# Performance work log

Hardware: AMD Instinct MI355X
Metric: run time of the kernel (lower is better)

## Reference

```python
import jax, jax.numpy as jnp
import numpy as np

EMBED_DIM = 768
NUM_HEADS = 12
HEAD_DIM = EMBED_DIM // NUM_HEADS


def setup_inputs() -> dict:
    key = jax.random.key(0)
    k_x, k_wqkv, k_bqkv, k_wo, k_bo = jax.random.split(key, 5)
    B, S, D = 4, 2048, EMBED_DIM
    bound = 1.0 / np.sqrt(D)
    x = jax.random.normal(k_x, (B, S, D), dtype=jnp.float32)
    # nn.Linear weights: torch stores [out, in]; we keep same layout and use x @ W.T
    W_qkv = jax.random.uniform(k_wqkv, (3 * D, D), jnp.float32, -bound, bound)
    b_qkv = jax.random.uniform(k_bqkv, (3 * D,), jnp.float32, -bound, bound)
    W_out = jax.random.uniform(k_wo, (D, D), jnp.float32, -bound, bound)
    b_out = jax.random.uniform(k_bo, (D,), jnp.float32, -bound, bound)
    return {"x": x, "W_qkv": W_qkv, "b_qkv": b_qkv, "W_out": W_out, "b_out": b_out}


def reference(x, W_qkv, b_qkv, W_out, b_out):
    B, S, D = x.shape
    H, Hd = NUM_HEADS, HEAD_DIM
    qkv = x @ W_qkv.T + b_qkv                       # [B,S,3D]
    qkv = qkv.reshape(B, S, H, 3 * Hd).transpose(0, 2, 1, 3)  # [B,H,S,3Hd]
    q, k, v = jnp.split(qkv, 3, axis=-1)            # each [B,H,S,Hd]
    scale = Hd ** -0.5
    scores = jnp.einsum("bhsd,bhtd->bhst", q, k) * scale  # [B,H,S,S]
    weights = jax.nn.softmax(scores, axis=-1)
    ctx = jnp.einsum("bhst,bhtd->bhsd", weights, v)       # [B,H,S,Hd]
    ctx = ctx.transpose(0, 2, 1, 3).reshape(B, S, D)      # [B,S,D]
    return ctx @ W_out.T + b_out
```

## Files before the change

kernel.cpp:

```cpp
#include <hip/hip_runtime.h>
#include <hip/hip_bf16.h>
#include <stdint.h>
#include <math.h>

typedef unsigned short u16;
typedef __attribute__((ext_vector_type(8))) short short8;
typedef __attribute__((ext_vector_type(4))) short short4v;
typedef __attribute__((ext_vector_type(4))) float f32x4;
typedef __attribute__((ext_vector_type(16))) float f32x16;
typedef __attribute__((ext_vector_type(4))) unsigned int u32x4;
typedef __attribute__((ext_vector_type(2))) unsigned int u32x2;

#define NB 4
#define NS 2048
#define NH 12
#define HD 64
#define ND 768
#define ND3 2304

#define QSCALE 0.18033688f

__device__ __forceinline__ u16 f2bf(float f) {
    unsigned int u = __float_as_uint(f);
    unsigned int r = u + 0x7fffu + ((u >> 16) & 1u);
    return (u16)(r >> 16);
}

__device__ __forceinline__ void gload16(const u16* g, u16* s) {
    __builtin_amdgcn_global_load_lds(
        (const __attribute__((address_space(1))) unsigned int*)(const void*)g,
        (__attribute__((address_space(3))) unsigned int*)(void*)s, 16, 0, 0);
}

#define XN4   1572864
#define WQN4  442368
#define WON4  147456
__global__ __launch_bounds__(256) void castall(const float* __restrict__ x,
                                               const float* __restrict__ wq,
                                               const float* __restrict__ wo,
                                               u16* __restrict__ xb,
                                               u16* __restrict__ wqb,
                                               u16* __restrict__ wob) {
    int i = blockIdx.x * 256 + threadIdx.x;
    const float* s; u16* d; int j;
    if (i < XN4) { s = x; d = xb; j = i; }
    else if (i < XN4 + WQN4) { s = wq; d = wqb; j = i - XN4; }
    else if (i < XN4 + WQN4 + WON4) { s = wo; d = wob; j = i - XN4 - WQN4; }
    else return;
    float4 v = ((const float4*)s)[j];
    ushort4 o;
    o.x = f2bf(v.x); o.y = f2bf(v.y); o.z = f2bf(v.z); o.w = f2bf(v.w);
    ((ushort4*)d)[j] = o;
}

__global__ __launch_bounds__(256, 3) void gemm_qkv(const u16* __restrict__ A,
                                                   const u16* __restrict__ Bw,
                                                   const float* __restrict__ bias,
                                                   u16* __restrict__ Qg,
                                                   u16* __restrict__ Kg,
                                                   u16* __restrict__ Vtg) {
    __shared__ u16 lds[2][10240];
    const int tid = threadIdx.x;
    const int w = tid >> 6, l = tid & 63;
    const int lam = l & 15, quad = l >> 4;
    const int wm = w >> 1, wn = w & 1;
    const int bm = blockIdx.x * 128;
    const int hh = blockIdx.y;
    const int bn = hh * 192;
    const int K = ND;

    f32x4 acc[4][6];
#pragma unroll
    for (int i = 0; i < 4; i++)
#pragma unroll
        for (int j = 0; j < 6; j++) { f32x4 z = {0.f, 0.f, 0.f, 0.f}; acc[i][j] = z; }

    const u16* gp[5];
    int so[5];
#pragma unroll
    for (int i = 0; i < 5; i++) {
        int c = w * 5 + i;
        if (c < 8) { gp[i] = A + (size_t)(bm + c * 16 + lam) * K + quad * 8; so[i] = c * 512; }
        else { int nf = c - 8; gp[i] = Bw + (size_t)(bn + nf * 16 + lam) * K + quad * 8; so[i] = 4096 + nf * 512; }
    }

#pragma unroll
    for (int i = 0; i < 5; i++) gload16(gp[i], &lds[0][so[i]]);
    asm volatile("s_waitcnt vmcnt(0)" ::: "memory");
    __syncthreads();

    int cur = 0;
    for (int k0 = 0; k0 < K; k0 += 32) {
        if (k0 + 32 < K) {
#pragma unroll
            for (int i = 0; i < 5; i++) gload16(gp[i] + k0 + 32, &lds[cur ^ 1][so[i]]);
        }
        short8 a[4];
#pragma unroll
        for (int i = 0; i < 4; i++) a[i] = *(const short8*)(&lds[cur][(wm * 4 + i) * 512 + l * 8]);
#pragma unroll
        for (int half = 0; half < 2; half++) {
            short8 b[3];
#pragma unroll
            for (int j = 0; j < 3; j++) b[j] = *(const short8*)(&lds[cur][4096 + (wn * 6 + half * 3 + j) * 512 + l * 8]);
#pragma unroll
            for (int mf = 0; mf < 4; mf++)
#pragma unroll
                for (int j = 0; j < 3; j++)
                    acc[mf][half * 3 + j] = __builtin_amdgcn_mfma_f32_16x16x32_bf16(a[mf], b[j], acc[mf][half * 3 + j], 0, 0, 0);
        }
        asm volatile("s_waitcnt vmcnt(0)" ::: "memory");
        __syncthreads();
        cur ^= 1;
    }

#pragma unroll
    for (int nf = 0; nf < 6; nf++) {
        int nloc = wn * 96 + nf * 16;
        int rgn = nloc / 64;
        int d = (nloc % 64) + lam;
        float bv = bias[bn + nloc + lam];
        if (rgn == 2) {
#pragma unroll
            for (int mf = 0; mf < 4; mf++) {
                int m0 = bm + wm * 64 + mf * 16 + quad * 4;
                int bq = m0 >> 11, s0 = m0 & 2047;
                ushort4 o;
                o.x = f2bf(acc[mf][nf][0] + bv);
                o.y = f2bf(acc[mf][nf][1] + bv);
                o.z = f2bf(acc[mf][nf][2] + bv);
                o.w = f2bf(acc[mf][nf][3] + bv);
                *(ushort4*)(Vtg + ((size_t)((bq * NH + hh) * HD + d)) * NS + s0) = o;
            }
        } else {
            u16* dst = (rgn == 0) ? Qg : Kg;
            const float sc = (rgn == 0) ? QSCALE : 1.0f;
#pragma unroll
            for (int mf = 0; mf < 4; mf++)
#pragma unroll
                for (int r = 0; r < 4; r++) {
                    int m = bm + wm * 64 + mf * 16 + quad * 4 + r;
                    int bq = m >> 11, s = m & 2047;
                    dst[((size_t)((bq * NH + hh) * NS + s)) * HD + d] = f2bf((acc[mf][nf][r] + bv) * sc);
                }
        }
    }
}

__global__ __launch_bounds__(256, 3) void attn(const u16* __restrict__ Qg,
                                               const u16* __restrict__ Kg,
                                               const u16* __restrict__ Vtg,
                                               u16* __restrict__ ctx) {
    __shared__ u16 kt_lds[8192];
    __shared__ u16 vt_lds[8192];
    __shared__ float linv[128];
    const int tid = threadIdx.x;
    const int w = tid >> 6, L = tid & 63;
    const int r5 = L & 31, h = L >> 5;
    const int bid = blockIdx.x;
    const int qt = bid / 48, bh = bid % 48;
    const int b = bh / NH, hd = bh % NH;
    const u16* Qh = Qg + (size_t)bh * NS * HD;
    const u16* Kh = Kg + (size_t)bh * NS * HD;
    const u16* Vh = Vtg + (size_t)bh * HD * NS;

    const int qbase = qt * 128 + w * 32;

    short8 qf[4];
#pragma unroll
    for (int s = 0; s < 4; s++)
        qf[s] = *(const short8*)(Qh + (size_t)(qbase + r5) * HD + s * 16 + h * 8);

    f32x16 ot[2];
#pragma unroll
    for (int hg = 0; hg < 2; hg++)
#pragma unroll
        for (int r = 0; r < 16; r++) ot[hg][r] = 0.f;
    float lacc = 0.f;

    const u16* gp[8];
    u16* sp[8];
    int step;
    if (w < 2) {
#pragma unroll
        for (int i = 0; i < 8; i++) {
            int c = w * 8 + i, kg = c >> 2, s = c & 3;
            gp[i] = Kh + (size_t)(kg * 32 + r5) * HD + s * 16 + h * 8;
            sp[i] = kt_lds + c * 512;
        }
        step = 128 * HD;
    } else {
#pragma unroll
        for (int i = 0; i < 8; i++) {
            int c = (w - 2) * 8 + i;
            gp[i] = Vh + (size_t)((c >> 3) * 32 + r5) * NS + (c & 7) * 16 + h * 8;
            sp[i] = vt_lds + c * 512;
        }
        step = 128;
    }

    u32x4 rg[8];
#pragma unroll
    for (int i = 0; i < 8; i++) { rg[i] = *(const u32x4*)gp[i]; gp[i] += step; }

    for (int kt = 0; kt < 16; kt++) {
        __syncthreads();
#pragma unroll
        for (int i = 0; i < 8; i++) *(u32x4*)(sp[i] + (size_t)L * 8) = rg[i];
        __syncthreads();

        if (kt < 15) {
#pragma unroll
            for (int i = 0; i < 8; i++) { rg[i] = *(const u32x4*)gp[i]; gp[i] += step; }
        }

#pragma unroll
        for (int kg = 0; kg < 4; kg++) {
            f32x16 st;
#pragma unroll
            for (int r = 0; r < 16; r++) st[r] = 0.f;
#pragma unroll
            for (int s = 0; s < 4; s++) {
                short8 kf = *(const short8*)(kt_lds + (kg * 4 + s) * 512 + L * 8);
                st = __builtin_amdgcn_mfma_f32_32x32x16_bf16(kf, qf[s], st, 0, 0, 0);
            }

            unsigned int q8[8];
#pragma unroll
            for (int i = 0; i < 8; i++) {
                float e0 = __builtin_amdgcn_exp2f(st[2 * i + 0]);
                float e1 = __builtin_amdgcn_exp2f(st[2 * i + 1]);
                lacc += e0 + e1;
                unsigned int u0 = __float_as_uint(e0) + 0x8000u;
                unsigned int u1 = __float_as_uint(e1) + 0x8000u;
                q8[i] = __builtin_amdgcn_perm(u1, u0, 0x07060302u);
            }
            u32x2 s02 = __builtin_amdgcn_permlane32_swap(q8[0], q8[2], false, false);
            u32x2 s13 = __builtin_amdgcn_permlane32_swap(q8[1], q8[3], false, false);
            u32x2 s46 = __builtin_amdgcn_permlane32_swap(q8[4], q8[6], false, false);
            u32x2 s57 = __builtin_amdgcn_permlane32_swap(q8[5], q8[7], false, false);
            union { u32x4 u; short8 s; } af0, af1;
            af0.u = (u32x4){s02.x, s13.x, s02.y, s13.y};
            af1.u = (u32x4){s46.x, s57.x, s46.y, s57.y};

#pragma unroll
            for (int hg = 0; hg < 2; hg++) {
                short8 vf0 = *(const short8*)(vt_lds + (hg * 8 + kg * 2 + 0) * 512 + L * 8);
                short8 vf1 = *(const short8*)(vt_lds + (hg * 8 + kg * 2 + 1) * 512 + L * 8);
                ot[hg] = __builtin_amdgcn_mfma_f32_32x32x16_bf16(af0.s, vf0, ot[hg], 0, 0, 0);
                ot[hg] = __builtin_amdgcn_mfma_f32_32x32x16_bf16(af1.s, vf1, ot[hg], 0, 0, 0);
            }
        }
    }

    float lg = lacc + __shfl_xor(lacc, 32);
    linv[w * 32 + r5] = 1.0f / lg;
    __builtin_amdgcn_s_waitcnt(0xc07f);

    float sc[16];
#pragma unroll
    for (int r = 0; r < 16; r++) sc[r] = linv[w * 32 + (r & 3) + 8 * (r >> 2) + 4 * h];
#pragma unroll
    for (int hg = 0; hg < 2; hg++) {
#pragma unroll
        for (int r = 0; r < 16; r++) {
            int q = qbase + (r & 3) + 8 * (r >> 2) + 4 * h;
            ctx[(size_t)(b * NS + q) * ND + hd * HD + hg * 32 + r5] = f2bf(ot[hg][r] * sc[r]);
        }
    }
}

__global__ __launch_bounds__(256) void gemm_out(const u16* __restrict__ A,
                                                const u16* __restrict__ Bw,
                                                const float* __restrict__ bias,
                                                float* __restrict__ out) {
    __shared__ u16 lds[2][7168];
    const int tid = threadIdx.x;
    const int w = tid >> 6, l = tid & 63;
    const int lam = l & 15, quad = l >> 4;
    const int wm = w >> 1, wn = w & 1;
    const int bm = blockIdx.x * 128, bn = blockIdx.y * 96;
    const int K = ND;

    f32x4 acc[4][3];
#pragma unroll
    for (int i = 0; i < 4; i++)
#pragma unroll
        for (int j = 0; j < 3; j++) { f32x4 z = {0.f, 0.f, 0.f, 0.f}; acc[i][j] = z; }

    const u16* gp[4];
    int so[4];
#pragma unroll
    for (int i = 0; i < 4; i++) {
        int c = w * 4 + i;
        if (c >= 14) c -= 14;
        if (c < 8) { gp[i] = A + (size_t)(bm + c * 16 + lam) * K + quad * 8; so[i] = c * 512; }
        else { int nf = c - 8; gp[i] = Bw + (size_t)(bn + nf * 16 + lam) * K + quad * 8; so[i] = 4096 + nf * 512; }
    }

#pragma unroll
    for (int i = 0; i < 4; i++) gload16(gp[i], &lds[0][so[i]]);
    asm volatile("s_waitcnt vmcnt(0)" ::: "memory");
    __syncthreads();

    int cur = 0;
    for (int k0 = 0; k0 < K; k0 += 32) {
        if (k0 + 32 < K) {
#pragma unroll
            for (int i = 0; i < 4; i++) gload16(gp[i] + k0 + 32, &lds[cur ^ 1][so[i]]);
        }
        short8 a[4], b[3];
#pragma unroll
        for (int i = 0; i < 4; i++) a[i] = *(const short8*)(&lds[cur][(wm * 4 + i) * 512 + l * 8]);
#pragma unroll
        for (int j = 0; j < 3; j++) b[j] = *(const short8*)(&lds[cur][4096 + (wn * 3 + j) * 512 + l * 8]);
#pragma unroll
        for (int mf = 0; mf < 4; mf++)
#pragma unroll
            for (int j = 0; j < 3; j++)
                acc[mf][j] = __builtin_amdgcn_mfma_f32_16x16x32_bf16(a[mf], b[j], acc[mf][j], 0, 0, 0);
        asm volatile("s_waitcnt vmcnt(0)" ::: "memory");
        __syncthreads();
        cur ^= 1;
    }

#pragma unroll
    for (int nf = 0; nf < 3; nf++) {
        int n = bn + wn * 48 + nf * 16 + lam;
        float bv = bias[n];
#pragma unroll
        for (int mf = 0; mf < 4; mf++)
#pragma unroll
            for (int r = 0; r < 4; r++) {
                int m = bm + wm * 64 + mf * 16 + quad * 4 + r;
                out[(size_t)m * ND + n] = acc[mf][nf][r] + bv;
            }
    }
}

extern "C" void kernel_launch(void* const* d_in, const int* in_sizes, int n_in,
                              void* d_out, int out_size, void* d_ws, size_t ws_size,
                              hipStream_t stream) {
    const float* x    = (const float*)d_in[0];
    const float* Wqkv = (const float*)d_in[1];
    const float* bqkv = (const float*)d_in[2];
    const float* Wout = (const float*)d_in[3];
    const float* bout = (const float*)d_in[4];
    float* out = (float*)d_out;

    u16* p = (u16*)d_ws;
    u16* xb    = p; p += 6291456;
    u16* wqkvb = p; p += 1769472;
    u16* wob   = p; p += 589824;
    u16* Qg    = p; p += 6291456;
    u16* Kg    = p; p += 6291456;
    u16* Vtg   = p; p += 6291456;
    u16* ctx   = p; p += 6291456;

    castall<<<8448, 256, 0, stream>>>(x, Wqkv, Wout, xb, wqkvb, wob);
    gemm_qkv<<<dim3(64, 12), 256, 0, stream>>>(xb, wqkvb, bqkv, Qg, Kg, Vtg);
    attn<<<768, 256, 0, stream>>>(Qg, Kg, Vtg, ctx);
    gemm_out<<<dim3(64, 8), 256, 0, stream>>>(ctx, wob, bout, out);
}
```

Measured before the change: 227.8 us.

## Compute softmax row sums via MFMA with ones, use hardware bf16 pack and setprio

The attention kernel now accumulates the softmax denominator with two extra MFMAs against a ones vector instead of scalar VALU adds, removing the cross-lane shuffle, the LDS linv buffer and its barrier-like wait. It also replaces manual round-and-perm bf16 packing with v_cvt_pk_bf16_f32, starts the QK accumulation from a pinned zero vector, and raises wave priority around the MFMA sections. This trades VALU work for extra matrix-core work (two more MFMAs per kg step) and 16 more accumulator registers, which could reduce occupancy. The denominator is now summed from bf16-rounded probabilities, which matches what is actually multiplied with V.

```diff
diff --git a/kernel.cpp b/kernel.cpp
--- a/kernel.cpp
+++ b/kernel.cpp
@@ -153,7 +153,6 @@
                                                u16* __restrict__ ctx) {
     __shared__ u16 kt_lds[8192];
     __shared__ u16 vt_lds[8192];
-    __shared__ float linv[128];
     const int tid = threadIdx.x;
     const int w = tid >> 6, L = tid & 63;
     const int r5 = L & 31, h = L >> 5;
@@ -176,7 +175,18 @@
     for (int hg = 0; hg < 2; hg++)
 #pragma unroll
         for (int r = 0; r < 16; r++) ot[hg][r] = 0.f;
-    float lacc = 0.f;
+
+    f32x16 lsum;
+#pragma unroll
+    for (int r = 0; r < 16; r++) lsum[r] = 0.f;
+    short8 onesf;
+#pragma unroll
+    for (int i = 0; i < 8; i++) onesf[i] = (short)0x3F80;
+
+    f32x16 zero16;
+#pragma unroll
+    for (int r = 0; r < 16; r++) zero16[r] = 0.f;
+    asm volatile("" : "+v"(zero16));
 
     const u16* gp[8];
     u16* sp[8];
@@ -216,24 +226,25 @@
 
 #pragma unroll
         for (int kg = 0; kg < 4; kg++) {
-            f32x16 st;
-#pragma unroll
-            for (int r = 0; r < 16; r++) st[r] = 0.f;
-#pragma unroll
-            for (int s = 0; s < 4; s++) {
+            __builtin_amdgcn_s_setprio(1);
+            short8 kf0 = *(const short8*)(kt_lds + (kg * 4 + 0) * 512 + L * 8);
+            f32x16 st = __builtin_amdgcn_mfma_f32_32x32x16_bf16(kf0, qf[0], zero16, 0, 0, 0);
+#pragma unroll
+            for (int s = 1; s < 4; s++) {
                 short8 kf = *(const short8*)(kt_lds + (kg * 4 + s) * 512 + L * 8);
                 st = __builtin_amdgcn_mfma_f32_32x32x16_bf16(kf, qf[s], st, 0, 0, 0);
             }
-
+            __builtin_amdgcn_s_setprio(0);
+
+            float e[16];
+#pragma unroll
+            for (int i = 0; i < 16; i++) e[i] = __builtin_amdgcn_exp2f(st[i]);
             unsigned int q8[8];
 #pragma unroll
             for (int i = 0; i < 8; i++) {
-                float e0 = __builtin_amdgcn_exp2f(st[2 * i + 0]);
-                float e1 = __builtin_amdgcn_exp2f(st[2 * i + 1]);
-                lacc += e0 + e1;
-                unsigned int u0 = __float_as_uint(e0) + 0x8000u;
-                unsigned int u1 = __float_as_uint(e1) + 0x8000u;
-                q8[i] = __builtin_amdgcn_perm(u1, u0, 0x07060302u);
+                unsigned int pk;
+                asm("v_cvt_pk_bf16_f32 %0, %1, %2" : "=v"(pk) : "v"(e[2 * i]), "v"(e[2 * i + 1]));
+                q8[i] = pk;
             }
             u32x2 s02 = __builtin_amdgcn_permlane32_swap(q8[0], q8[2], false, false);
             u32x2 s13 = __builtin_amdgcn_permlane32_swap(q8[1], q8[3], false, false);
@@ -243,6 +254,9 @@
             af0.u = (u32x4){s02.x, s13.x, s02.y, s13.y};
             af1.u = (u32x4){s46.x, s57.x, s46.y, s57.y};
 
+            __builtin_amdgcn_s_setprio(1);
+            lsum = __builtin_amdgcn_mfma_f32_32x32x16_bf16(af0.s, onesf, lsum, 0, 0, 0);
+            lsum = __builtin_amdgcn_mfma_f32_32x32x16_bf16(af1.s, onesf, lsum, 0, 0, 0);
 #pragma unroll
             for (int hg = 0; hg < 2; hg++) {
                 short8 vf0 = *(const short8*)(vt_lds + (hg * 8 + kg * 2 + 0) * 512 + L * 8);
@@ -250,22 +264,19 @@
                 ot[hg] = __builtin_amdgcn_mfma_f32_32x32x16_bf16(af0.s, vf0, ot[hg], 0, 0, 0);
                 ot[hg] = __builtin_amdgcn_mfma_f32_32x32x16_bf16(af1.s, vf1, ot[hg], 0, 0, 0);
             }
-        }
-    }
-
-    float lg = lacc + __shfl_xor(lacc, 32);
-    linv[w * 32 + r5] = 1.0f / lg;
-    __builtin_amdgcn_s_waitcnt(0xc07f);
-
-    float sc[16];
-#pragma unroll
-    for (int r = 0; r < 16; r++) sc[r] = linv[w * 32 + (r & 3) + 8 * (r >> 2) + 4 * h];
+            __builtin_amdgcn_s_setprio(0);
+        }
+    }
+
+    float inv[16];
+#pragma unroll
+    for (int r = 0; r < 16; r++) inv[r] = __builtin_amdgcn_rcpf(lsum[r]);
 #pragma unroll
     for (int hg = 0; hg < 2; hg++) {
 #pragma unroll
         for (int r = 0; r < 16; r++) {
             int q = qbase + (r & 3) + 8 * (r >> 2) + 4 * h;
-            ctx[(size_t)(b * NS + q) * ND + hd * HD + hg * 32 + r5] = f2bf(ot[hg][r] * sc[r]);
+            ctx[(size_t)(b * NS + q) * ND + hd * HD + hg * 32 + r5] = f2bf(ot[hg][r] * inv[r]);
         }
     }
 }
```

After: 224.5 us. About the same (-1.5%).
